# Kernel optimization log

Measured on AMD Instinct MI355X. Metric: run time of the kernel, lower is better.

## Reference

```python
import jax, jax.numpy as jnp
import numpy as np

N = 8192
F_IN = 1024
F_OUT = 256
ALPHA = 0.2          # LeakyReLU negative slope
ADJ_DENSITY = 0.004  # pre-symmetrization edge probability -> avg degree ~65
NEG_INF = -9.0e15    # matches -9000000000000000.0 in the torch code


def setup_inputs() -> dict:
    key = jax.random.key(0)
    k_h, k_W, k_a, k_adj = jax.random.split(key, 4)
    h = jax.random.normal(k_h, (N, F_IN), dtype=jnp.float32)
    # xavier_uniform with gain=1.414
    lim_W = 1.414 * np.sqrt(6.0 / (F_IN + F_OUT))
    W = jax.random.uniform(k_W, (F_IN, F_OUT), dtype=jnp.float32, minval=-lim_W, maxval=lim_W)
    lim_a = 1.414 * np.sqrt(6.0 / (2 * F_OUT + 1))
    a = jax.random.uniform(k_a, (2 * F_OUT, 1), dtype=jnp.float32, minval=-lim_a, maxval=lim_a)
    # sparse symmetric 0/1 adjacency (float, like the torch code's dense adj)
    u = jax.random.uniform(k_adj, (N, N))
    m = u < ADJ_DENSITY
    adj = (m | m.T).astype(jnp.float32)
    return {"h": h, "adj": adj, "W": W, "a": a}


def reference(h, adj, W, a):
    # --- GAT attention ---
    Wh = h @ W                                   # [N, F_OUT]
    Wh1 = Wh @ a[:F_OUT]                          # [N, 1]
    Wh2 = Wh @ a[F_OUT:]                          # [N, 1]
    e = jax.nn.leaky_relu(Wh1 + Wh2.T, negative_slope=ALPHA)   # [N, N]
    attention = jax.nn.softmax(jnp.where(adj > 0, e, NEG_INF), axis=1)

    # --- per-row variable-k pruning of attention + attention@attention.T ---
    n = adj.shape[0]
    diag = jnp.eye(n, dtype=bool)
    adj_nodiag = jnp.where(diag, 0.0, adj)
    s2 = jnp.count_nonzero(adj_nodiag, axis=1)    # [N] int, variable k per row

    attention2step = attention @ attention.T      # [N, N] dense GEMM
    comb = attention + attention2step
    comb = jnp.where(diag, 0.0, comb)

    # threshold = s2[i]-th largest value of row i (np.partition(row, -k)[-k])
    sorted_desc = -jnp.sort(-comb, axis=1)        # [N, N] descending per row
    idx = jnp.maximum(s2 - 1, 0)[:, None]         # clamp for s2==0 rows
    thr = jnp.take_along_axis(sorted_desc, idx, axis=1)   # [N, 1]
    # keep values >= threshold (torch code zeros values strictly < partition);
    # rows with s2 == 0 are zeroed entirely
    pruned = jnp.where((s2[:, None] > 0) & (comb >= thr), comb, 0.0)
    adj_resize = (pruned > 0).astype(jnp.float32)

    # --- output (eval mode: dropout is identity); concat=True -> ELU ---
    h_prime = attention @ Wh                      # [N, F_OUT]
    return jax.nn.elu(h_prime), adj_resize
```

## Files before the change

kernel.cpp:

```cpp
#include <hip/hip_runtime.h>
#include <cstdint>
#include <cstddef>

#define NN 8192
#define KFIN 1024
#define KFOUT 256
#define MAXD 192
#define LRALPHA 0.2f

typedef float f32x4 __attribute__((ext_vector_type(4)));

__global__ void __launch_bounds__(256) k_build_csr(
    const float* __restrict__ adj, int* __restrict__ nbr,
    int* __restrict__ deg, int* __restrict__ s2v) {
  const int wave = threadIdx.x >> 6;
  const int lane = threadIdx.x & 63;
  const int row = blockIdx.x * 4 + wave;
  const float* arow = adj + (size_t)row * NN;
  int* outp = nbr + (size_t)row * MAXD;
  int count = 0;
  int dflag = 0;
  const unsigned long long below = (1ull << lane) - 1ull;
  for (int c0 = 0; c0 < NN; c0 += 256) {
    const int c = c0 + lane * 4;
    const f32x4 v = __builtin_nontemporal_load(
        reinterpret_cast<const f32x4*>(arow + c));
    const unsigned long long m0 = __ballot(v[0] > 0.0f);
    const unsigned long long m1 = __ballot(v[1] > 0.0f);
    const unsigned long long m2 = __ballot(v[2] > 0.0f);
    const unsigned long long m3 = __ballot(v[3] > 0.0f);
    int pos = count + (int)(__popcll(m0 & below) + __popcll(m1 & below) +
                            __popcll(m2 & below) + __popcll(m3 & below));
    if (v[0] > 0.0f) { if (pos < MAXD) outp[pos] = c + 0; ++pos; if (c + 0 == row) dflag = 1; }
    if (v[1] > 0.0f) { if (pos < MAXD) outp[pos] = c + 1; ++pos; if (c + 1 == row) dflag = 1; }
    if (v[2] > 0.0f) { if (pos < MAXD) outp[pos] = c + 2; ++pos; if (c + 2 == row) dflag = 1; }
    if (v[3] > 0.0f) { if (pos < MAXD) outp[pos] = c + 3; ++pos; if (c + 3 == row) dflag = 1; }
    count += (int)(__popcll(m0) + __popcll(m1) + __popcll(m2) + __popcll(m3));
  }
  const int anyd = __any(dflag) ? 1 : 0;
  if (lane == 0) {
    deg[row] = count < MAXD ? count : MAXD;
    s2v[row] = count - anyd;
  }
}

__global__ void __launch_bounds__(256) k_gemm(
    const float* __restrict__ A, const float* __restrict__ B,
    float* __restrict__ C) {
  __shared__ float As[32][65];
  __shared__ float Bs[32][65];
  const int tid = threadIdx.x;
  const int brow = blockIdx.y * 64;
  const int bcol = blockIdx.x * 64;
  const int tx = tid & 15;
  const int ty = tid >> 4;
  float acc[4][4];
#pragma unroll
  for (int i = 0; i < 4; ++i)
#pragma unroll
    for (int j = 0; j < 4; ++j) acc[i][j] = 0.0f;
  const int ar = tid >> 2;
  const int ac = (tid & 3) << 2;
  const int br = tid >> 4;
  const int bc = (tid & 15) << 2;
  for (int k0 = 0; k0 < KFIN; k0 += 32) {
    const float4 av0 =
        *reinterpret_cast<const float4*>(A + (size_t)(brow + ar) * KFIN + k0 + ac);
    const float4 av1 =
        *reinterpret_cast<const float4*>(A + (size_t)(brow + ar) * KFIN + k0 + 16 + ac);
    const float4 bv0 =
        *reinterpret_cast<const float4*>(B + (size_t)(k0 + br) * KFOUT + bcol + bc);
    const float4 bv1 =
        *reinterpret_cast<const float4*>(B + (size_t)(k0 + 16 + br) * KFOUT + bcol + bc);
    As[ac + 0][ar] = av0.x;
    As[ac + 1][ar] = av0.y;
    As[ac + 2][ar] = av0.z;
    As[ac + 3][ar] = av0.w;
    As[16 + ac + 0][ar] = av1.x;
    As[16 + ac + 1][ar] = av1.y;
    As[16 + ac + 2][ar] = av1.z;
    As[16 + ac + 3][ar] = av1.w;
    Bs[br][bc + 0] = bv0.x;
    Bs[br][bc + 1] = bv0.y;
    Bs[br][bc + 2] = bv0.z;
    Bs[br][bc + 3] = bv0.w;
    Bs[16 + br][bc + 0] = bv1.x;
    Bs[16 + br][bc + 1] = bv1.y;
    Bs[16 + br][bc + 2] = bv1.z;
    Bs[16 + br][bc + 3] = bv1.w;
    __syncthreads();
#pragma unroll
    for (int kk = 0; kk < 32; ++kk) {
      const float a0 = As[kk][ty * 4 + 0];
      const float a1 = As[kk][ty * 4 + 1];
      const float a2 = As[kk][ty * 4 + 2];
      const float a3 = As[kk][ty * 4 + 3];
      const float b0 = Bs[kk][tx * 4 + 0];
      const float b1 = Bs[kk][tx * 4 + 1];
      const float b2 = Bs[kk][tx * 4 + 2];
      const float b3 = Bs[kk][tx * 4 + 3];
      acc[0][0] += a0 * b0; acc[0][1] += a0 * b1; acc[0][2] += a0 * b2; acc[0][3] += a0 * b3;
      acc[1][0] += a1 * b0; acc[1][1] += a1 * b1; acc[1][2] += a1 * b2; acc[1][3] += a1 * b3;
      acc[2][0] += a2 * b0; acc[2][1] += a2 * b1; acc[2][2] += a2 * b2; acc[2][3] += a2 * b3;
      acc[3][0] += a3 * b0; acc[3][1] += a3 * b1; acc[3][2] += a3 * b2; acc[3][3] += a3 * b3;
    }
    __syncthreads();
  }
#pragma unroll
  for (int i = 0; i < 4; ++i) {
#pragma unroll
    for (int j = 0; j < 4; ++j) {
      C[(size_t)(brow + ty * 4 + i) * KFOUT + bcol + tx * 4 + j] = acc[i][j];
    }
  }
}

__global__ void __launch_bounds__(256) k_rowdots(
    const float* __restrict__ Wh, const float* __restrict__ a,
    float* __restrict__ Wh1, float* __restrict__ Wh2) {
  const int wave = threadIdx.x >> 6;
  const int lane = threadIdx.x & 63;
  const int row = blockIdx.x * 4 + wave;
  const float4 w = *reinterpret_cast<const float4*>(Wh + (size_t)row * KFOUT + lane * 4);
  const float4 aA = *reinterpret_cast<const float4*>(a + lane * 4);
  const float4 aB = *reinterpret_cast<const float4*>(a + KFOUT + lane * 4);
  float sA = w.x * aA.x + w.y * aA.y + w.z * aA.z + w.w * aA.w;
  float sB = w.x * aB.x + w.y * aB.y + w.z * aB.z + w.w * aB.w;
  for (int o = 32; o > 0; o >>= 1) {
    sA += __shfl_xor(sA, o);
    sB += __shfl_xor(sB, o);
  }
  if (lane == 0) {
    Wh1[row] = sA;
    Wh2[row] = sB;
  }
}

__global__ void __launch_bounds__(256) k_stats(
    const int* __restrict__ nbr, const int* __restrict__ deg,
    const float* __restrict__ Wh1, const float* __restrict__ Wh2,
    float2* __restrict__ mz, float* __restrict__ att,
    short* __restrict__ qb8) {
  const int wave = threadIdx.x >> 6;
  const int lane = threadIdx.x & 63;
  const int row = blockIdx.x * 4 + wave;
  const int d = deg[row];
  const size_t rowbase = (size_t)row * MAXD;
  const int* cols = nbr + rowbase;
  const float w1 = Wh1[row];
  int c0 = 0x7fffffff, c1 = 0x7fffffff, c2 = 0x7fffffff;
  float e0 = -1e30f, e1 = -1e30f, e2 = -1e30f;
  const bool a0 = lane < d, a1 = lane + 64 < d, a2 = lane + 128 < d;
  if (a0) { c0 = cols[lane];       float x = w1 + Wh2[c0]; e0 = x > 0.0f ? x : LRALPHA * x; }
  if (a1) { c1 = cols[lane + 64];  float x = w1 + Wh2[c1]; e1 = x > 0.0f ? x : LRALPHA * x; }
  if (a2) { c2 = cols[lane + 128]; float x = w1 + Wh2[c2]; e2 = x > 0.0f ? x : LRALPHA * x; }
  float mx = fmaxf(e0, fmaxf(e1, e2));
  for (int o = 32; o > 0; o >>= 1) mx = fmaxf(mx, __shfl_xor(mx, o));
  const float x0 = a0 ? expf(e0 - mx) : 0.0f;
  const float x1 = a1 ? expf(e1 - mx) : 0.0f;
  const float x2 = a2 ? expf(e2 - mx) : 0.0f;
  float sum = x0 + x1 + x2;
  for (int o = 32; o > 0; o >>= 1) sum += __shfl_xor(sum, o);
  const float Z = (d > 0) ? sum : 1.0f;
  const float invZ = 1.0f / Z;
  if (a0) att[rowbase + lane] = x0 * invZ;
  if (a1) att[rowbase + lane + 64] = x1 * invZ;
  if (a2) att[rowbase + lane + 128] = x2 * invZ;
  int b[7] = {0, 0, 0, 0, 0, 0, 0};
#pragma unroll
  for (int m = 1; m <= 7; ++m) {
    b[m - 1] = (int)__popcll(__ballot(a0 && c0 < m * 1024)) +
               (int)__popcll(__ballot(a1 && c1 < m * 1024)) +
               (int)__popcll(__ballot(a2 && c2 < m * 1024));
  }
  if (lane == 0) {
    mz[row] = make_float2(mx, invZ);
    short* q = qb8 + (size_t)row * 8;
    q[0] = (short)b[0]; q[1] = (short)b[1]; q[2] = (short)b[2]; q[3] = (short)b[3];
    q[4] = (short)b[4]; q[5] = (short)b[5]; q[6] = (short)b[6]; q[7] = (short)d;
  }
}

__global__ void __launch_bounds__(256) k_att(
    const int* __restrict__ nbr, const int* __restrict__ deg,
    const float* __restrict__ Wh1, const float* __restrict__ Wh2,
    const float2* __restrict__ mz, const float* __restrict__ att,
    const float* __restrict__ Wh, int2* __restrict__ edgesT,
    float* __restrict__ out0) {
  const int wave = threadIdx.x >> 6;
  const int lane = threadIdx.x & 63;
  const int row = blockIdx.x * 4 + wave;
  const int d = deg[row];
  const size_t rowbase = (size_t)row * MAXD;
  const int* cols = nbr + rowbase;
  const float w2r = Wh2[row];
  for (int t = lane; t < d; t += 64) {
    const int j = cols[t];
    float e2 = Wh1[j] + w2r;
    e2 = e2 > 0.0f ? e2 : LRALPHA * e2;
    const float2 m = mz[j];
    const float v = expf(e2 - m.x) * m.y;
    edgesT[rowbase + t] = make_int2(j, __float_as_int(v));
  }
  {
    const float* arow = att + rowbase;
    f32x4 p0 = {0, 0, 0, 0}, p1 = {0, 0, 0, 0};
    f32x4 p2 = {0, 0, 0, 0}, p3 = {0, 0, 0, 0};
    int t = 0;
    for (; t + 3 < d; t += 4) {
      const int j0 = cols[t], j1 = cols[t + 1], j2 = cols[t + 2], j3 = cols[t + 3];
      const float w0 = arow[t], w1 = arow[t + 1], w2 = arow[t + 2], w3 = arow[t + 3];
      const f32x4 a0 = *reinterpret_cast<const f32x4*>(Wh + (size_t)j0 * KFOUT + lane * 4);
      const f32x4 a1 = *reinterpret_cast<const f32x4*>(Wh + (size_t)j1 * KFOUT + lane * 4);
      const f32x4 a2 = *reinterpret_cast<const f32x4*>(Wh + (size_t)j2 * KFOUT + lane * 4);
      const f32x4 a3 = *reinterpret_cast<const f32x4*>(Wh + (size_t)j3 * KFOUT + lane * 4);
      p0 += w0 * a0;
      p1 += w1 * a1;
      p2 += w2 * a2;
      p3 += w3 * a3;
    }
    for (; t < d; ++t) {
      const int j = cols[t];
      const float w = arow[t];
      p0 += w * *reinterpret_cast<const f32x4*>(Wh + (size_t)j * KFOUT + lane * 4);
    }
    const f32x4 r = (p0 + p1) + (p2 + p3);
    f32x4 o;
    o[0] = r[0] > 0.0f ? r[0] : expm1f(r[0]);
    o[1] = r[1] > 0.0f ? r[1] : expm1f(r[1]);
    o[2] = r[2] > 0.0f ? r[2] : expm1f(r[2]);
    o[3] = r[3] > 0.0f ? r[3] : expm1f(r[3]);
    __builtin_nontemporal_store(
        o, reinterpret_cast<f32x4*>(&out0[(size_t)row * KFOUT + lane * 4]));
  }
}

__global__ void __launch_bounds__(512) k_twostep(
    const int* __restrict__ nbr, const int* __restrict__ deg,
    const int* __restrict__ s2v, const float* __restrict__ att,
    const int2* __restrict__ edgesT, const short* __restrict__ qb8,
    float* __restrict__ out1) {
  __shared__ float comb[NN];
  __shared__ float wvals[MAXD];
  __shared__ unsigned short kcols[MAXD];
  __shared__ short sqb[MAXD][8];
  __shared__ unsigned int hist[256];
  __shared__ unsigned int scomp[512];
  __shared__ unsigned int shPrefix;
  __shared__ int shRemaining;
  __shared__ int shNc;
  const int tid = threadIdx.x;
  const int wave = tid >> 6;
  const int lane = tid & 63;
  const int row = blockIdx.x;
  const f32x4 z4 = {0.0f, 0.0f, 0.0f, 0.0f};
  for (int j = tid * 4; j < NN; j += 2048)
    *reinterpret_cast<f32x4*>(&comb[j]) = z4;
  const int d = deg[row];
  const int* cols = nbr + (size_t)row * MAXD;
  const float* arow = att + (size_t)row * MAXD;
  for (int t = tid; t < d; t += 512) {
    const int c = cols[t];
    kcols[t] = (unsigned short)c;
    wvals[t] = arow[t];
    *reinterpret_cast<int4*>(&sqb[t][0]) =
        *reinterpret_cast<const int4*>(&qb8[(size_t)c * 8]);
  }
  if (tid == 0) shNc = 0;
  __syncthreads();
  {
    const int grp = lane >> 3;
    const int sub = lane & 7;
    for (int t0 = 0; t0 < d; t0 += 8) {
      const int t = t0 + grp;
      if (t < d) {
        const int qs = wave ? (int)sqb[t][wave - 1] : 0;
        const int qe = (int)sqb[t][wave];
        const float w = wvals[t];
        const int2* ek = edgesT + (size_t)kcols[t] * MAXD;
        for (int off = qs + sub; off < qe; off += 8) {
          const int2 e = ek[off];
          atomicAdd(&comb[e.x], w * __int_as_float(e.y));
        }
      }
    }
  }
  {
    const short* qr = qb8 + (size_t)row * 8;
    const int qlo = wave ? (int)qr[wave - 1] : 0;
    const int qhi = (int)qr[wave];
    for (int t = qlo + lane; t < qhi; t += 64) comb[(int)kcols[t]] += wvals[t];
  }
  __syncthreads();
  if (tid == 0) comb[row] = 0.0f;
  __syncthreads();
  const int kk = s2v[row];
  const size_t obase = (size_t)row * NN;
  if (kk <= 0) {
    for (int j = tid * 4; j < NN; j += 2048)
      __builtin_nontemporal_store(z4, reinterpret_cast<f32x4*>(&out1[obase + j]));
    return;
  }
  if (tid < 256) hist[tid] = 0u;
  __syncthreads();
  for (int j = tid * 4; j < NN; j += 2048) {
    const f32x4 cv = *reinterpret_cast<const f32x4*>(&comb[j]);
#pragma unroll
    for (int q = 0; q < 4; ++q) {
      const unsigned int u = __float_as_uint(cv[q]);
      if (u != 0u) atomicAdd(&hist[u >> 24], 1u);
    }
  }
  __syncthreads();
  if (tid < 64) {
    const int bHi = 255 - 4 * lane;
    const unsigned int c0 = hist[bHi];
    const unsigned int c1 = hist[bHi - 1];
    const unsigned int c2 = hist[bHi - 2];
    const unsigned int c3 = hist[bHi - 3];
    const unsigned int gs = c0 + c1 + c2 + c3;
    unsigned int run2 = gs;
    for (int o = 1; o < 64; o <<= 1) {
      const unsigned int tt = __shfl_up(run2, o);
      if (lane >= o) run2 += tt;
    }
    const unsigned int pre = run2 - gs;
    const unsigned int rem = (unsigned int)kk;
    if (pre < rem && pre + gs >= rem) {
      unsigned int above;
      int digit;
      if (pre + c0 >= rem) { digit = bHi; above = pre; }
      else if (pre + c0 + c1 >= rem) { digit = bHi - 1; above = pre + c0; }
      else if (pre + c0 + c1 + c2 >= rem) { digit = bHi - 2; above = pre + c0 + c1; }
      else { digit = bHi - 3; above = pre + c0 + c1 + c2; }
      shPrefix = (unsigned)digit << 24;
      shRemaining = kk - (int)above;
    }
  }
  __syncthreads();
  unsigned int prefix = shPrefix;
  int remaining = shRemaining;
  const unsigned int digit0 = prefix >> 24;
  __syncthreads();
  for (int j = tid * 4; j < NN; j += 2048) {
    const f32x4 cv = *reinterpret_cast<const f32x4*>(&comb[j]);
#pragma unroll
    for (int q = 0; q < 4; ++q) {
      const unsigned int u = __float_as_uint(cv[q]);
      if (u != 0u && (u >> 24) == digit0) {
        const int idx = atomicAdd(&shNc, 1);
        if (idx < 512) scomp[idx] = u;
      }
    }
  }
  __syncthreads();
  const int nc = shNc;
  const bool densefb = nc > 512;
  const unsigned int myu = (!densefb && tid < nc) ? scomp[tid] : 0u;
  for (int pass = 1; pass < 4; ++pass) {
    const int shift = 24 - 8 * pass;
    const unsigned int pmask = 0xFFFFFFFFu << (shift + 8);
    if (tid < 256) hist[tid] = 0u;
    __syncthreads();
    if (!densefb) {
      if (tid < nc && (myu & pmask) == prefix)
        atomicAdd(&hist[(myu >> shift) & 255u], 1u);
    } else {
      for (int j = tid * 4; j < NN; j += 2048) {
        const f32x4 cv = *reinterpret_cast<const f32x4*>(&comb[j]);
#pragma unroll
        for (int q = 0; q < 4; ++q) {
          const unsigned int u = __float_as_uint(cv[q]);
          if (u != 0u && (u & pmask) == prefix)
            atomicAdd(&hist[(u >> shift) & 255u], 1u);
        }
      }
    }
    __syncthreads();
    if (tid < 64) {
      const int bHi = 255 - 4 * lane;
      const unsigned int c0 = hist[bHi];
      const unsigned int c1 = hist[bHi - 1];
      const unsigned int c2 = hist[bHi - 2];
      const unsigned int c3 = hist[bHi - 3];
      const unsigned int gs = c0 + c1 + c2 + c3;
      unsigned int run2 = gs;
      for (int o = 1; o < 64; o <<= 1) {
        const unsigned int tt = __shfl_up(run2, o);
        if (lane >= o) run2 += tt;
      }
      const unsigned int pre = run2 - gs;
      const unsigned int rem = (unsigned int)remaining;
      if (pre < rem && pre + gs >= rem) {
        unsigned int above;
        int digit;
        if (pre + c0 >= rem) { digit = bHi; above = pre; }
        else if (pre + c0 + c1 >= rem) { digit = bHi - 1; above = pre + c0; }
        else if (pre + c0 + c1 + c2 >= rem) { digit = bHi - 2; above = pre + c0 + c1; }
        else { digit = bHi - 3; above = pre + c0 + c1 + c2; }
        shPrefix = prefix | ((unsigned int)digit << shift);
        shRemaining = remaining - (int)above;
      }
    }
    __syncthreads();
    prefix = shPrefix;
    remaining = shRemaining;
    __syncthreads();
  }
  const float thr = __uint_as_float(prefix);
  for (int j = tid * 4; j < NN; j += 2048) {
    const f32x4 cv = *reinterpret_cast<const f32x4*>(&comb[j]);
    f32x4 ov;
    ov[0] = (cv[0] >= thr && cv[0] > 0.0f) ? 1.0f : 0.0f;
    ov[1] = (cv[1] >= thr && cv[1] > 0.0f) ? 1.0f : 0.0f;
    ov[2] = (cv[2] >= thr && cv[2] > 0.0f) ? 1.0f : 0.0f;
    ov[3] = (cv[3] >= thr && cv[3] > 0.0f) ? 1.0f : 0.0f;
    __builtin_nontemporal_store(ov, reinterpret_cast<f32x4*>(&out1[obase + j]));
  }
}

extern "C" void kernel_launch(void* const* d_in, const int* in_sizes, int n_in,
                              void* d_out, int out_size, void* d_ws, size_t ws_size,
                              hipStream_t stream) {
  const float* h = (const float*)d_in[0];
  const float* adj = (const float*)d_in[1];
  const float* W = (const float*)d_in[2];
  const float* a = (const float*)d_in[3];

  float* out0 = (float*)d_out;
  float* out1 = out0 + (size_t)NN * KFOUT;

  float* Wh = (float*)d_ws;
  float* Wh1 = Wh + (size_t)NN * KFOUT;
  float* Wh2 = Wh1 + NN;
  float* mrow = Wh2 + NN;
  float* Zrow = mrow + NN;
  float* att = Zrow + NN;
  float* edgesF = att + (size_t)NN * MAXD;
  int2* edgesT = (int2*)edgesF;
  int* nbr = (int*)(edgesF + (size_t)NN * MAXD * 2);
  int* deg = nbr + (size_t)NN * MAXD;
  int* s2v = deg + NN;
  short* qb8 = (short*)(s2v + NN);
  float2* mz = (float2*)(qb8 + (size_t)NN * 8);

  k_build_csr<<<NN / 4, 256, 0, stream>>>(adj, nbr, deg, s2v);
  dim3 ggrid(KFOUT / 64, NN / 64);
  k_gemm<<<ggrid, 256, 0, stream>>>(h, W, Wh);
  k_rowdots<<<NN / 4, 256, 0, stream>>>(Wh, a, Wh1, Wh2);
  k_stats<<<NN / 4, 256, 0, stream>>>(nbr, deg, Wh1, Wh2, mz, att, qb8);
  k_att<<<NN / 4, 256, 0, stream>>>(nbr, deg, Wh1, Wh2, mz, att, Wh, edgesT, out0);
  k_twostep<<<NN, 512, 0, stream>>>(nbr, deg, s2v, att, edgesT, qb8, out1);
}
```

Before: 462.3 us.

## Fuse CSR build into softmax stats kernel and gather Wh as bf16

Merges the adjacency-scan CSR construction into the per-row softmax stats kernel, which removes one launch and one global re-read of the neighbor lists. The per-1024-column bucket counts are now recorded during the scan instead of being recomputed with ballots. The GEMM also writes a bf16 copy of Wh when workspace allows, and the attention aggregation gathers that half-width copy to cut gather bandwidth. The cost is bf16 rounding error in the output and an extra store in the GEMM.

After: 452.2 us. 1.02x faster.

```diff
diff --git a/kernel.cpp b/kernel.cpp
--- a/kernel.cpp
+++ b/kernel.cpp
@@ -10,43 +10,17 @@
 
 typedef float f32x4 __attribute__((ext_vector_type(4)));
 
-__global__ void __launch_bounds__(256) k_build_csr(
-    const float* __restrict__ adj, int* __restrict__ nbr,
-    int* __restrict__ deg, int* __restrict__ s2v) {
-  const int wave = threadIdx.x >> 6;
-  const int lane = threadIdx.x & 63;
-  const int row = blockIdx.x * 4 + wave;
-  const float* arow = adj + (size_t)row * NN;
-  int* outp = nbr + (size_t)row * MAXD;
-  int count = 0;
-  int dflag = 0;
-  const unsigned long long below = (1ull << lane) - 1ull;
-  for (int c0 = 0; c0 < NN; c0 += 256) {
-    const int c = c0 + lane * 4;
-    const f32x4 v = __builtin_nontemporal_load(
-        reinterpret_cast<const f32x4*>(arow + c));
-    const unsigned long long m0 = __ballot(v[0] > 0.0f);
-    const unsigned long long m1 = __ballot(v[1] > 0.0f);
-    const unsigned long long m2 = __ballot(v[2] > 0.0f);
-    const unsigned long long m3 = __ballot(v[3] > 0.0f);
-    int pos = count + (int)(__popcll(m0 & below) + __popcll(m1 & below) +
-                            __popcll(m2 & below) + __popcll(m3 & below));
-    if (v[0] > 0.0f) { if (pos < MAXD) outp[pos] = c + 0; ++pos; if (c + 0 == row) dflag = 1; }
-    if (v[1] > 0.0f) { if (pos < MAXD) outp[pos] = c + 1; ++pos; if (c + 1 == row) dflag = 1; }
-    if (v[2] > 0.0f) { if (pos < MAXD) outp[pos] = c + 2; ++pos; if (c + 2 == row) dflag = 1; }
-    if (v[3] > 0.0f) { if (pos < MAXD) outp[pos] = c + 3; ++pos; if (c + 3 == row) dflag = 1; }
-    count += (int)(__popcll(m0) + __popcll(m1) + __popcll(m2) + __popcll(m3));
-  }
-  const int anyd = __any(dflag) ? 1 : 0;
-  if (lane == 0) {
-    deg[row] = count < MAXD ? count : MAXD;
-    s2v[row] = count - anyd;
-  }
+__device__ __forceinline__ unsigned short bf16_rne(float x) {
+  const unsigned u = __float_as_uint(x);
+  return (unsigned short)((u + 0x7FFFu + ((u >> 16) & 1u)) >> 16);
+}
+__device__ __forceinline__ float bf16_to_f32(unsigned short b) {
+  return __uint_as_float((unsigned)b << 16);
 }
 
 __global__ void __launch_bounds__(256) k_gemm(
     const float* __restrict__ A, const float* __restrict__ B,
-    float* __restrict__ C) {
+    float* __restrict__ C, unsigned short* __restrict__ Cb) {
   __shared__ float As[32][65];
   __shared__ float Bs[32][65];
   const int tid = threadIdx.x;
@@ -110,7 +84,9 @@
   for (int i = 0; i < 4; ++i) {
 #pragma unroll
     for (int j = 0; j < 4; ++j) {
-      C[(size_t)(brow + ty * 4 + i) * KFOUT + bcol + tx * 4 + j] = acc[i][j];
+      const size_t idx = (size_t)(brow + ty * 4 + i) * KFOUT + bcol + tx * 4 + j;
+      C[idx] = acc[i][j];
+      if (Cb) Cb[idx] = bf16_rne(acc[i][j]);
     }
   }
 }
@@ -136,24 +112,60 @@
   }
 }
 
-__global__ void __launch_bounds__(256) k_stats(
-    const int* __restrict__ nbr, const int* __restrict__ deg,
-    const float* __restrict__ Wh1, const float* __restrict__ Wh2,
+__global__ void __launch_bounds__(256) k_csr_stats(
+    const float* __restrict__ adj, const float* __restrict__ Wh1,
+    const float* __restrict__ Wh2, int* __restrict__ nbr,
+    int* __restrict__ deg, int* __restrict__ s2v,
     float2* __restrict__ mz, float* __restrict__ att,
     short* __restrict__ qb8) {
   const int wave = threadIdx.x >> 6;
   const int lane = threadIdx.x & 63;
   const int row = blockIdx.x * 4 + wave;
-  const int d = deg[row];
+  const float* arow = adj + (size_t)row * NN;
+  int* outp = nbr + (size_t)row * MAXD;
+  int count = 0;
+  int dflag = 0;
+  int b[7];
+  const unsigned long long below = (1ull << lane) - 1ull;
+  for (int c0 = 0; c0 < NN; c0 += 256) {
+    if (c0 > 0 && (c0 & 1023) == 0) b[(c0 >> 10) - 1] = count;
+    const int c = c0 + lane * 4;
+    const f32x4 v = __builtin_nontemporal_load(
+        reinterpret_cast<const f32x4*>(arow + c));
+    const unsigned long long m0 = __ballot(v[0] > 0.0f);
+    const unsigned long long m1 = __ballot(v[1] > 0.0f);
+    const unsigned long long m2 = __ballot(v[2] > 0.0f);
+    const unsigned long long m3 = __ballot(v[3] > 0.0f);
+    int pos = count + (int)(__popcll(m0 & below) + __popcll(m1 & below) +
+                            __popcll(m2 & below) + __popcll(m3 & below));
+    if (v[0] > 0.0f) { if (pos < MAXD) outp[pos] = c + 0; ++pos; if (c + 0 == row) dflag = 1; }
+    if (v[1] > 0.0f) { if (pos < MAXD) outp[pos] = c + 1; ++pos; if (c + 1 == row) dflag = 1; }
+    if (v[2] > 0.0f) { if (pos < MAXD) outp[pos] = c + 2; ++pos; if (c + 2 == row) dflag = 1; }
+    if (v[3] > 0.0f) { if (pos < MAXD) outp[pos] = c + 3; ++pos; if (c + 3 == row) dflag = 1; }
+    count += (int)(__popcll(m0) + __popcll(m1) + __popcll(m2) + __popcll(m3));
+  }
+  const int anyd = __any(dflag) ? 1 : 0;
+  const int d = count < MAXD ? count : MAXD;
+  if (lane == 0) {
+    deg[row] = d;
+    s2v[row] = count - anyd;
+    short* q = qb8 + (size_t)row * 8;
+#pragma unroll
+    for (int w = 0; w < 7; ++w) {
+      const int bw = b[w] < d ? b[w] : d;
+      q[w] = (short)bw;
+    }
+    q[7] = (short)d;
+  }
   const size_t rowbase = (size_t)row * MAXD;
-  const int* cols = nbr + rowbase;
+  const int* cols = outp;
   const float w1 = Wh1[row];
-  int c0 = 0x7fffffff, c1 = 0x7fffffff, c2 = 0x7fffffff;
+  int c0i = 0x7fffffff, c1i = 0x7fffffff, c2i = 0x7fffffff;
   float e0 = -1e30f, e1 = -1e30f, e2 = -1e30f;
   const bool a0 = lane < d, a1 = lane + 64 < d, a2 = lane + 128 < d;
-  if (a0) { c0 = cols[lane];       float x = w1 + Wh2[c0]; e0 = x > 0.0f ? x : LRALPHA * x; }
-  if (a1) { c1 = cols[lane + 64];  float x = w1 + Wh2[c1]; e1 = x > 0.0f ? x : LRALPHA * x; }
-  if (a2) { c2 = cols[lane + 128]; float x = w1 + Wh2[c2]; e2 = x > 0.0f ? x : LRALPHA * x; }
+  if (a0) { c0i = cols[lane];       float x = w1 + Wh2[c0i]; e0 = x > 0.0f ? x : LRALPHA * x; }
+  if (a1) { c1i = cols[lane + 64];  float x = w1 + Wh2[c1i]; e1 = x > 0.0f ? x : LRALPHA * x; }
+  if (a2) { c2i = cols[lane + 128]; float x = w1 + Wh2[c2i]; e2 = x > 0.0f ? x : LRALPHA * x; }
   float mx = fmaxf(e0, fmaxf(e1, e2));
   for (int o = 32; o > 0; o >>= 1) mx = fmaxf(mx, __shfl_xor(mx, o));
   const float x0 = a0 ? expf(e0 - mx) : 0.0f;
@@ -166,27 +178,15 @@
   if (a0) att[rowbase + lane] = x0 * invZ;
   if (a1) att[rowbase + lane + 64] = x1 * invZ;
   if (a2) att[rowbase + lane + 128] = x2 * invZ;
-  int b[7] = {0, 0, 0, 0, 0, 0, 0};
-#pragma unroll
-  for (int m = 1; m <= 7; ++m) {
-    b[m - 1] = (int)__popcll(__ballot(a0 && c0 < m * 1024)) +
-               (int)__popcll(__ballot(a1 && c1 < m * 1024)) +
-               (int)__popcll(__ballot(a2 && c2 < m * 1024));
-  }
-  if (lane == 0) {
-    mz[row] = make_float2(mx, invZ);
-    short* q = qb8 + (size_t)row * 8;
-    q[0] = (short)b[0]; q[1] = (short)b[1]; q[2] = (short)b[2]; q[3] = (short)b[3];
-    q[4] = (short)b[4]; q[5] = (short)b[5]; q[6] = (short)b[6]; q[7] = (short)d;
-  }
+  if (lane == 0) mz[row] = make_float2(mx, invZ);
 }
 
 __global__ void __launch_bounds__(256) k_att(
     const int* __restrict__ nbr, const int* __restrict__ deg,
     const float* __restrict__ Wh1, const float* __restrict__ Wh2,
     const float2* __restrict__ mz, const float* __restrict__ att,
-    const float* __restrict__ Wh, int2* __restrict__ edgesT,
-    float* __restrict__ out0) {
+    const float* __restrict__ Wh, const unsigned short* __restrict__ Whb,
+    int2* __restrict__ edgesT, float* __restrict__ out0) {
   const int wave = threadIdx.x >> 6;
   const int lane = threadIdx.x & 63;
   const int row = blockIdx.x * 4 + wave;
@@ -207,22 +207,48 @@
     f32x4 p0 = {0, 0, 0, 0}, p1 = {0, 0, 0, 0};
     f32x4 p2 = {0, 0, 0, 0}, p3 = {0, 0, 0, 0};
     int t = 0;
-    for (; t + 3 < d; t += 4) {
-      const int j0 = cols[t], j1 = cols[t + 1], j2 = cols[t + 2], j3 = cols[t + 3];
-      const float w0 = arow[t], w1 = arow[t + 1], w2 = arow[t + 2], w3 = arow[t + 3];
-      const f32x4 a0 = *reinterpret_cast<const f32x4*>(Wh + (size_t)j0 * KFOUT + lane * 4);
-      const f32x4 a1 = *reinterpret_cast<const f32x4*>(Wh + (size_t)j1 * KFOUT + lane * 4);
-      const f32x4 a2 = *reinterpret_cast<const f32x4*>(Wh + (size_t)j2 * KFOUT + lane * 4);
-      const f32x4 a3 = *reinterpret_cast<const f32x4*>(Wh + (size_t)j3 * KFOUT + lane * 4);
-      p0 += w0 * a0;
-      p1 += w1 * a1;
-      p2 += w2 * a2;
-      p3 += w3 * a3;
-    }
-    for (; t < d; ++t) {
-      const int j = cols[t];
-      const float w = arow[t];
-      p0 += w * *reinterpret_cast<const f32x4*>(Wh + (size_t)j * KFOUT + lane * 4);
+    if (Whb) {
+      for (; t + 3 < d; t += 4) {
+        const int j0 = cols[t], j1 = cols[t + 1], j2 = cols[t + 2], j3 = cols[t + 3];
+        const float w0 = arow[t], w1 = arow[t + 1], w2 = arow[t + 2], w3 = arow[t + 3];
+        const ushort4 b0 = *reinterpret_cast<const ushort4*>(Whb + (size_t)j0 * KFOUT + lane * 4);
+        const ushort4 b1 = *reinterpret_cast<const ushort4*>(Whb + (size_t)j1 * KFOUT + lane * 4);
+        const ushort4 b2 = *reinterpret_cast<const ushort4*>(Whb + (size_t)j2 * KFOUT + lane * 4);
+        const ushort4 b3 = *reinterpret_cast<const ushort4*>(Whb + (size_t)j3 * KFOUT + lane * 4);
+        const f32x4 a0 = {bf16_to_f32(b0.x), bf16_to_f32(b0.y), bf16_to_f32(b0.z), bf16_to_f32(b0.w)};
+        const f32x4 a1 = {bf16_to_f32(b1.x), bf16_to_f32(b1.y), bf16_to_f32(b1.z), bf16_to_f32(b1.w)};
+        const f32x4 a2 = {bf16_to_f32(b2.x), bf16_to_f32(b2.y), bf16_to_f32(b2.z), bf16_to_f32(b2.w)};
+        const f32x4 a3 = {bf16_to_f32(b3.x), bf16_to_f32(b3.y), bf16_to_f32(b3.z), bf16_to_f32(b3.w)};
+        p0 += w0 * a0;
+        p1 += w1 * a1;
+        p2 += w2 * a2;
+        p3 += w3 * a3;
+      }
+      for (; t < d; ++t) {
+        const int j = cols[t];
+        const float w = arow[t];
+        const ushort4 b = *reinterpret_cast<const ushort4*>(Whb + (size_t)j * KFOUT + lane * 4);
+        const f32x4 av = {bf16_to_f32(b.x), bf16_to_f32(b.y), bf16_to_f32(b.z), bf16_to_f32(b.w)};
+        p0 += w * av;
+      }
+    } else {
+      for (; t + 3 < d; t += 4) {
+        const int j0 = cols[t], j1 = cols[t + 1], j2 = cols[t + 2], j3 = cols[t + 3];
+        const float w0 = arow[t], w1 = arow[t + 1], w2 = arow[t + 2], w3 = arow[t + 3];
+        const f32x4 a0 = *reinterpret_cast<const f32x4*>(Wh + (size_t)j0 * KFOUT + lane * 4);
+        const f32x4 a1 = *reinterpret_cast<const f32x4*>(Wh + (size_t)j1 * KFOUT + lane * 4);
+        const f32x4 a2 = *reinterpret_cast<const f32x4*>(Wh + (size_t)j2 * KFOUT + lane * 4);
+        const f32x4 a3 = *reinterpret_cast<const f32x4*>(Wh + (size_t)j3 * KFOUT + lane * 4);
+        p0 += w0 * a0;
+        p1 += w1 * a1;
+        p2 += w2 * a2;
+        p3 += w3 * a3;
+      }
+      for (; t < d; ++t) {
+        const int j = cols[t];
+        const float w = arow[t];
+        p0 += w * *reinterpret_cast<const f32x4*>(Wh + (size_t)j * KFOUT + lane * 4);
+      }
     }
     const f32x4 r = (p0 + p1) + (p2 + p3);
     f32x4 o;
@@ -443,12 +469,18 @@
   int* s2v = deg + NN;
   short* qb8 = (short*)(s2v + NN);
   float2* mz = (float2*)(qb8 + (size_t)NN * 8);
-
-  k_build_csr<<<NN / 4, 256, 0, stream>>>(adj, nbr, deg, s2v);
+  unsigned short* Whb = (unsigned short*)(mz + NN);
+  const size_t need =
+      (size_t)((char*)(Whb + (size_t)NN * KFOUT) - (char*)d_ws);
+  const bool useB = ws_size >= need;
+  unsigned short* WhbArg = useB ? Whb : nullptr;
+
   dim3 ggrid(KFOUT / 64, NN / 64);
-  k_gemm<<<ggrid, 256, 0, stream>>>(h, W, Wh);
+  k_gemm<<<ggrid, 256, 0, stream>>>(h, W, Wh, WhbArg);
   k_rowdots<<<NN / 4, 256, 0, stream>>>(Wh, a, Wh1, Wh2);
-  k_stats<<<NN / 4, 256, 0, stream>>>(nbr, deg, Wh1, Wh2, mz, att, qb8);
-  k_att<<<NN / 4, 256, 0, stream>>>(nbr, deg, Wh1, Wh2, mz, att, Wh, edgesT, out0);
+  k_csr_stats<<<NN / 4, 256, 0, stream>>>(adj, Wh1, Wh2, nbr, deg, s2v, mz,
+                                          att, qb8);
+  k_att<<<NN / 4, 256, 0, stream>>>(nbr, deg, Wh1, Wh2, mz, att, Wh, WhbArg,
+                                    edgesT, out0);
   k_twostep<<<NN, 512, 0, stream>>>(nbr, deg, s2v, att, edgesT, qb8, out1);
 }
```
